# Optimization experiments

Hardware: AMD Instinct MI355X
Metric: run time of the kernel (lower is better)

The kernel has to match this reference:

```python
import jax, jax.numpy as jnp
import numpy as np

D_MODEL = 4096
NUM_EXPERTS = 16
HID_PER_EXPERT = 11008 // NUM_EXPERTS  # 688
NUM_SELECTS = 4
BALANCE_WEIGHT = 0.01
CV_EPS = 1e-10


def setup_inputs() -> dict:
    key = jax.random.key(0)
    ks = jax.random.split(key, 5)
    x = jax.random.normal(ks[0], (2, 2048, D_MODEL), dtype=jnp.float32)
    # gate network: Linear(input_size, num_experts, bias=False); stored as [D, E] for x @ W
    w_gate_net = jax.random.normal(ks[1], (D_MODEL, NUM_EXPERTS), dtype=jnp.float32) * (1.0 / np.sqrt(D_MODEL))
    # per-expert GLU weights (torch Linear convention [out, in]), stacked over experts
    s = 1.0 / np.sqrt(D_MODEL)
    w_g = jax.random.normal(ks[2], (NUM_EXPERTS, HID_PER_EXPERT, D_MODEL), dtype=jnp.float32) * s
    w_u = jax.random.normal(ks[3], (NUM_EXPERTS, HID_PER_EXPERT, D_MODEL), dtype=jnp.float32) * s
    w_d = jax.random.normal(ks[4], (NUM_EXPERTS, D_MODEL, HID_PER_EXPERT), dtype=jnp.float32) * (1.0 / np.sqrt(HID_PER_EXPERT))
    return {"x": x, "w_gate_net": w_gate_net, "w_g": w_g, "w_u": w_u, "w_d": w_d}


def _cv_squared(v):
    v = v.astype(jnp.float32)
    return jnp.var(v, ddof=1) / (jnp.mean(v) ** 2 + CV_EPS)


def reference(x, w_gate_net, w_g, w_u, w_d):
    B, S, D = x.shape
    E = w_g.shape[0]
    xt = x.reshape(-1, D)                      # [T, D]
    T = xt.shape[0]

    # --- TopKBalancedNoisyGate (eval path: no noise) ---
    logits = xt @ w_gate_net                   # [T, E]
    top_logits, top_idx = jax.lax.top_k(logits, NUM_SELECTS)   # [T, K]
    scores = jax.nn.softmax(top_logits.astype(jnp.float32), axis=-1).astype(logits.dtype)
    combine = jnp.zeros((T, E), dtype=logits.dtype)
    combine = combine.at[jnp.arange(T)[:, None], top_idx].set(scores)  # scatter topK scores
    importance = combine.sum(axis=0)           # [E]
    load = (combine > 0).sum(axis=0).astype(jnp.float32)
    balance_loss = (_cv_squared(importance) + _cv_squared(load)) * BALANCE_WEIGHT

    # --- UniversalCalculator with LinearGLUExperts (silu GLU, no bias) ---
    # dense per-expert compute; unrouted tokens have combine weight 0, so math matches
    # the gather/grouped-GEMM/scatter of the original exactly.
    g = jnp.einsum('td,ehd->teh', xt, w_g)     # [T, E, Hper]
    u = jnp.einsum('td,ehd->teh', xt, w_u)
    h = jax.nn.silu(g) * u * combine[:, :, None]  # multiply_gate_scores before down proj (bias-free => exact)
    y = jnp.einsum('teh,edh->td', h, w_d)      # [T, D]
    return y.reshape(B, S, -1), balance_loss
```

## Files before the change

kernel.cpp:

```cpp
#include <hip/hip_runtime.h>
#include <hip/hip_bf16.h>

#define D_MODEL 4096
#define NEXP    16
#define HID     688
#define HIDP    704
#define NSEL    4
#define NTOK    4096

typedef __attribute__((ext_vector_type(4))) float  f32x4;
typedef __attribute__((ext_vector_type(8))) short  bf16x8;

__device__ __forceinline__ short f2bf(float f) {
  __hip_bfloat16 h = __float2bfloat16(f);
  return __builtin_bit_cast(short, h);
}

__device__ __forceinline__ void gload16(const void* g, void* l) {
  __builtin_amdgcn_global_load_lds(
      (const __attribute__((address_space(1))) unsigned int*)g,
      (__attribute__((address_space(3))) unsigned int*)l, 16, 0, 0);
}

__global__ void zero_meta_kernel(int* counts, float* importance) {
  const int tid = threadIdx.x;
  if (tid < NEXP) counts[tid] = 0;
  else if (tid < 2 * NEXP) importance[tid - NEXP] = 0.f;
}

__global__ void zero_y_kernel(float* __restrict__ y) {
  const size_t i = (size_t)blockIdx.x * 256 + threadIdx.x;
  *(f32x4*)(y + i * 4) = f32x4{0.f, 0.f, 0.f, 0.f};
}

#define GC_CONV_BLOCKS 2048
__global__ __launch_bounds__(256) void gate_conv_kernel(
    const float* __restrict__ x, const float* __restrict__ wg,
    int* __restrict__ counts, float* __restrict__ importance,
    int* __restrict__ pair_tok, float* __restrict__ pair_scr,
    int* __restrict__ pair_rank, short* __restrict__ xb,
    const float* __restrict__ w_g, const float* __restrict__ w_u,
    short* __restrict__ gb, short* __restrict__ ub)
{
  __shared__ double red[4][NEXP];
  const int tid = threadIdx.x;

  if (blockIdx.x < GC_CONV_BLOCKS) {
    const size_t stride = (size_t)GC_CONV_BLOCKS * 256;
    const size_t n8 = (size_t)NEXP * HIDP * (D_MODEL / 8);
    for (size_t i = (size_t)blockIdx.x * 256 + tid; i < n8; i += stride) {
      const int c8  = (int)(i & 511);
      const int row = (int)((i >> 9) % HIDP);
      const int e   = (int)(i / (512 * HIDP));
      bf16x8 og, ou;
      if (row < HID) {
        const size_t so = ((size_t)e * HID + row) * D_MODEL + (size_t)c8 * 8;
        const f32x4 ga  = *(const f32x4*)(w_g + so);
        const f32x4 gbv = *(const f32x4*)(w_g + so + 4);
        const f32x4 ua  = *(const f32x4*)(w_u + so);
        const f32x4 ubv = *(const f32x4*)(w_u + so + 4);
        #pragma unroll
        for (int j = 0; j < 4; ++j) {
          og[j] = f2bf(ga[j]); og[4 + j] = f2bf(gbv[j]);
          ou[j] = f2bf(ua[j]); ou[4 + j] = f2bf(ubv[j]);
        }
      } else {
        #pragma unroll
        for (int j = 0; j < 8; ++j) { og[j] = 0; ou[j] = 0; }
      }
      *(bf16x8*)(gb + i * 8) = og;
      *(bf16x8*)(ub + i * 8) = ou;
    }
    return;
  }

  const int t = blockIdx.x - GC_CONV_BLOCKS;
  const float* xr = x + (size_t)t * D_MODEL;
  {
    short* xbr = xb + (size_t)t * D_MODEL;
    for (int i8 = tid; i8 < D_MODEL / 8; i8 += 256) {
      const f32x4 a = *(const f32x4*)(xr + i8 * 8);
      const f32x4 b = *(const f32x4*)(xr + i8 * 8 + 4);
      bf16x8 o;
      #pragma unroll
      for (int j = 0; j < 4; ++j) { o[j] = f2bf(a[j]); o[4 + j] = f2bf(b[j]); }
      *(bf16x8*)(xbr + i8 * 8) = o;
    }
  }

  double acc[NEXP];
  #pragma unroll
  for (int e = 0; e < NEXP; ++e) acc[e] = 0.0;

  for (int i = tid; i < D_MODEL; i += 256) {
    const float xv = xr[i];
    const f32x4* w = (const f32x4*)(wg + (size_t)i * NEXP);
    #pragma unroll
    for (int q = 0; q < 4; ++q) {
      const f32x4 wv = w[q];
      #pragma unroll
      for (int j = 0; j < 4; ++j) acc[q * 4 + j] += (double)xv * (double)wv[j];
    }
  }

  #pragma unroll
  for (int e = 0; e < NEXP; ++e) {
    double v = acc[e];
    #pragma unroll
    for (int off = 32; off > 0; off >>= 1) v += __shfl_xor(v, off, 64);
    acc[e] = v;
  }

  const int lane = tid & 63, wid = tid >> 6;
  if (lane == 0) {
    #pragma unroll
    for (int e = 0; e < NEXP; ++e) red[wid][e] = acc[e];
  }
  __syncthreads();

  if (tid == 0) {
    float lg[NEXP];
    #pragma unroll
    for (int e = 0; e < NEXP; ++e)
      lg[e] = (float)(red[0][e] + red[1][e] + red[2][e] + red[3][e]);

    int   idx[NSEL];
    float val[NSEL];
    unsigned used = 0;
    for (int k = 0; k < NSEL; ++k) {
      float best = -3.4e38f; int bi = 0;
      for (int e = 0; e < NEXP; ++e)
        if (!((used >> e) & 1u) && lg[e] > best) { best = lg[e]; bi = e; }
      idx[k] = bi; val[k] = best; used |= 1u << bi;
    }
    const float m = val[0];
    float ex[NSEL], s = 0.f;
    for (int k = 0; k < NSEL; ++k) { ex[k] = expf(val[k] - m); s += ex[k]; }
    for (int k = 0; k < NSEL; ++k) {
      const float sc = ex[k] / s;
      const int e = idx[k];
      const int pos = atomicAdd(&counts[e], 1);
      pair_tok[e * NTOK + pos]  = t;
      pair_scr[e * NTOK + pos]  = sc;
      pair_rank[e * NTOK + pos] = k;
      atomicAdd(&importance[e], sc);
    }
  }
}

__global__ void scan_loss_kernel(const int* __restrict__ counts,
                                 const float* __restrict__ importance,
                                 int* __restrict__ offs, float* __restrict__ loss_out)
{
  if (threadIdx.x != 0 || blockIdx.x != 0) return;
  int   c[NEXP]; float im[NEXP];
  for (int e = 0; e < NEXP; ++e) { c[e] = counts[e]; im[e] = importance[e]; }
  int o = 0;
  for (int e = 0; e < NEXP; ++e) { offs[e] = o; o += c[e]; }
  float mi = 0.f, ml = 0.f;
  for (int e = 0; e < NEXP; ++e) { mi += im[e]; ml += (float)c[e]; }
  mi /= NEXP; ml /= NEXP;
  float vi = 0.f, vl = 0.f;
  for (int e = 0; e < NEXP; ++e) {
    vi += (im[e] - mi) * (im[e] - mi);
    vl += ((float)c[e] - ml) * ((float)c[e] - ml);
  }
  vi /= (NEXP - 1); vl /= (NEXP - 1);
  const float loss = 0.01f * (vi / (mi * mi + 1e-10f) + vl / (ml * ml + 1e-10f));
  *loss_out = loss;
}

#define S1_CONV_BLOCKS 2048
__global__ __launch_bounds__(256, 4) void stage1_wd_kernel(
    const short* __restrict__ xb, const short* __restrict__ wgb,
    const short* __restrict__ wub, const int* __restrict__ counts,
    const int* __restrict__ offs, const int* __restrict__ pair_tok,
    const float* __restrict__ pair_scr, short* __restrict__ H,
    const float* __restrict__ w_d, short* __restrict__ wdb)
{
  __shared__ short ldsA[2][128 * 32];
  __shared__ short ldsG[2][64 * 32];
  __shared__ short ldsU[2][64 * 32];

  const int tid = threadIdx.x;

  if (blockIdx.x < S1_CONV_BLOCKS) {
    const size_t stride = (size_t)S1_CONV_BLOCKS * 256;
    const size_t n8 = (size_t)NEXP * D_MODEL * (HIDP / 8);
    for (size_t i = (size_t)blockIdx.x * 256 + tid; i < n8; i += stride) {
      const int c8  = (int)(i % 88);
      const int row = (int)((i / 88) & (D_MODEL - 1));
      const int e   = (int)(i / (88 * D_MODEL));
      bf16x8 o;
      if (c8 < 86) {
        const size_t so = ((size_t)e * D_MODEL + row) * HID + (size_t)c8 * 8;
        const f32x4 a = *(const f32x4*)(w_d + so);
        const f32x4 b = *(const f32x4*)(w_d + so + 4);
        #pragma unroll
        for (int j = 0; j < 4; ++j) { o[j] = f2bf(a[j]); o[4 + j] = f2bf(b[j]); }
      } else {
        #pragma unroll
        for (int j = 0; j < 8; ++j) o[j] = 0;
      }
      *(bf16x8*)(wdb + i * 8) = o;
    }
    return;
  }

  const int bid = blockIdx.x - S1_CONV_BLOCKS;
  const int ht  = bid >> 9;
  const int q   = bid & 511;
  const int xcd = q & 7;
  const int idx = q >> 3;
  const int e   = xcd * 2 + (idx & 1);
  const int mt  = idx >> 1;

  const int n_e = counts[e];
  const int m0  = mt * 128;
  if (m0 >= n_e) return;
  const int h0  = ht * 64;

  const int lane = tid & 63;
  const int wid  = tid >> 6;

  const short* srcA[2]; const short* srcG; const short* srcU;
  #pragma unroll
  for (int i = 0; i < 2; ++i) {
    const int c    = wid * 2 + i;
    const int row  = 16 * c + (lane >> 2);
    const int slot = (lane & 3) ^ ((row >> 1) & 3);
    int r = m0 + row; if (r >= n_e) r = n_e - 1;
    const int tok = pair_tok[e * NTOK + r];
    srcA[i] = xb + (size_t)tok * D_MODEL + slot * 8;
  }
  {
    const int c    = wid;
    const int row  = 16 * c + (lane >> 2);
    const int slot = (lane & 3) ^ ((row >> 1) & 3);
    const size_t rb = ((size_t)e * HIDP + h0 + row) * D_MODEL + slot * 8;
    srcG = wgb + rb;
    srcU = wub + rb;
  }

  const int wm = wid >> 1, wn = wid & 1;
  const int fr = lane & 15, fs = lane >> 4;
  const int so = (fs ^ ((fr >> 1) & 3)) * 8;

  f32x4 accg[4][2], accu[4][2];
  #pragma unroll
  for (int fi = 0; fi < 4; ++fi)
    #pragma unroll
    for (int fj = 0; fj < 2; ++fj) {
      accg[fi][fj] = f32x4{0.f, 0.f, 0.f, 0.f};
      accu[fi][fj] = f32x4{0.f, 0.f, 0.f, 0.f};
    }

  auto stage = [&](int kt, int b) {
    const int ko = kt * 32;
    #pragma unroll
    for (int i = 0; i < 2; ++i)
      gload16(srcA[i] + ko, &ldsA[b][(wid * 2 + i) * 512]);
    gload16(srcG + ko, &ldsG[b][wid * 512]);
    gload16(srcU + ko, &ldsU[b][wid * 512]);
  };

  auto compute = [&](int b) {
    const short* Ab = ldsA[b]; const short* Gb = ldsG[b]; const short* Ub = ldsU[b];
    bf16x8 af[4], bg[2], bu[2];
    #pragma unroll
    for (int fi = 0; fi < 4; ++fi)
      af[fi] = *(const bf16x8*)&Ab[(wm * 64 + fi * 16 + fr) * 32 + so];
    #pragma unroll
    for (int fj = 0; fj < 2; ++fj) {
      bg[fj] = *(const bf16x8*)&Gb[(wn * 32 + fj * 16 + fr) * 32 + so];
      bu[fj] = *(const bf16x8*)&Ub[(wn * 32 + fj * 16 + fr) * 32 + so];
    }
    #pragma unroll
    for (int fi = 0; fi < 4; ++fi)
      #pragma unroll
      for (int fj = 0; fj < 2; ++fj) {
        accg[fi][fj] = __builtin_amdgcn_mfma_f32_16x16x32_bf16(af[fi], bg[fj], accg[fi][fj], 0, 0, 0);
        accu[fi][fj] = __builtin_amdgcn_mfma_f32_16x16x32_bf16(af[fi], bu[fj], accu[fi][fj], 0, 0, 0);
      }
  };

  const int KT = D_MODEL / 32;
  stage(0, 0);
  for (int kt = 0; kt < KT; ++kt) {
    const int cur = kt & 1;
    __syncthreads();
    if (kt + 1 < KT) stage(kt + 1, cur ^ 1);
    compute(cur);
  }

  const int offs_e = offs[e];
  #pragma unroll
  for (int fi = 0; fi < 4; ++fi)
    #pragma unroll
    for (int fj = 0; fj < 2; ++fj)
      #pragma unroll
      for (int j = 0; j < 4; ++j) {
        const int r = m0 + wm * 64 + fi * 16 + fs * 4 + j;
        if (r < n_e) {
          const int c = h0 + wn * 32 + fj * 16 + fr;
          const float sc = pair_scr[e * NTOK + r];
          const float g  = accg[fi][fj][j];
          const float u  = accu[fi][fj][j];
          const float hv = (g / (1.f + expf(-g))) * u * sc;
          H[(size_t)(offs_e + r) * HIDP + c] = f2bf(hv);
        }
      }
}

__global__ __launch_bounds__(256, 4) void stage2s_kernel(
    const short* __restrict__ H, const short* __restrict__ wdb,
    const int* __restrict__ counts, const int* __restrict__ offs,
    const int* __restrict__ pair_tok, const int* __restrict__ pair_rank,
    float* __restrict__ Yk)
{
  const int bid = blockIdx.x;
  const int dt  = bid >> 9;
  const int q   = bid & 511;
  const int xcd = q & 7;
  const int idx = q >> 3;
  const int e   = xcd * 2 + (idx & 1);
  const int mt  = idx >> 1;

  const int n_e = counts[e];
  const int m0  = mt * 128;
  if (m0 >= n_e) return;
  const int d0  = dt * 128;

  __shared__ short ldsA[2][128 * 32];
  __shared__ short ldsB[2][128 * 32];

  const int tid  = threadIdx.x;
  const int lane = tid & 63;
  const int wid  = tid >> 6;
  const int offs_e = offs[e];

  const short* srcA[2]; const short* srcB[2];
  #pragma unroll
  for (int i = 0; i < 2; ++i) {
    const int c    = wid * 2 + i;
    const int row  = 16 * c + (lane >> 2);
    const int slot = (lane & 3) ^ ((row >> 1) & 3);
    int r = m0 + row; if (r >= n_e) r = n_e - 1;
    srcA[i] = H + (size_t)(offs_e + r) * HIDP + slot * 8;
    srcB[i] = wdb + ((size_t)e * D_MODEL + d0 + row) * HIDP + slot * 8;
  }

  const int wm = wid >> 1, wn = wid & 1;
  const int fr = lane & 15, fs = lane >> 4;
  const int so = (fs ^ ((fr >> 1) & 3)) * 8;

  f32x4 acc[4][4];
  #pragma unroll
  for (int fi = 0; fi < 4; ++fi)
    #pragma unroll
    for (int fj = 0; fj < 4; ++fj) acc[fi][fj] = f32x4{0.f, 0.f, 0.f, 0.f};

  auto stage = [&](int kt, int b) {
    const int ko = kt * 32;
    #pragma unroll
    for (int i = 0; i < 2; ++i) {
      gload16(srcA[i] + ko, &ldsA[b][(wid * 2 + i) * 512]);
      gload16(srcB[i] + ko, &ldsB[b][(wid * 2 + i) * 512]);
    }
  };

  auto compute = [&](int b) {
    const short* Ab = ldsA[b]; const short* Bb = ldsB[b];
    bf16x8 af[4], bb[4];
    #pragma unroll
    for (int fi = 0; fi < 4; ++fi)
      af[fi] = *(const bf16x8*)&Ab[(wm * 64 + fi * 16 + fr) * 32 + so];
    #pragma unroll
    for (int fj = 0; fj < 4; ++fj)
      bb[fj] = *(const bf16x8*)&Bb[(wn * 64 + fj * 16 + fr) * 32 + so];
    #pragma unroll
    for (int fi = 0; fi < 4; ++fi)
      #pragma unroll
      for (int fj = 0; fj < 4; ++fj)
        acc[fi][fj] = __builtin_amdgcn_mfma_f32_16x16x32_bf16(af[fi], bb[fj], acc[fi][fj], 0, 0, 0);
  };

  const int KT = HIDP / 32;
  stage(0, 0);
  for (int kt = 0; kt < KT; ++kt) {
    const int cur = kt & 1;
    __syncthreads();
    if (kt + 1 < KT) stage(kt + 1, cur ^ 1);
    compute(cur);
  }

  #pragma unroll
  for (int fi = 0; fi < 4; ++fi)
    #pragma unroll
    for (int j = 0; j < 4; ++j) {
      const int r = m0 + wm * 64 + fi * 16 + fs * 4 + j;
      if (r < n_e) {
        const int tok = pair_tok[e * NTOK + r];
        const int rk  = pair_rank[e * NTOK + r];
        float* yr = Yk + ((size_t)rk * NTOK + tok) * D_MODEL + d0 + wn * 64 + fr;
        #pragma unroll
        for (int fj = 0; fj < 4; ++fj)
          yr[fj * 16] = acc[fi][fj][j];
      }
    }
}

__global__ __launch_bounds__(256) void reduce_y_kernel(const float* __restrict__ Yk,
                                                       float* __restrict__ y) {
  const size_t i = ((size_t)blockIdx.x * 256 + threadIdx.x) * 4;
  const size_t P = (size_t)NTOK * D_MODEL;
  f32x4 s = *(const f32x4*)(Yk + i);
  s += *(const f32x4*)(Yk + P + i);
  s += *(const f32x4*)(Yk + 2 * P + i);
  s += *(const f32x4*)(Yk + 3 * P + i);
  *(f32x4*)(y + i) = s;
}

__global__ __launch_bounds__(256, 4) void stage2a_kernel(
    const short* __restrict__ H, const short* __restrict__ wdb,
    const int* __restrict__ counts, const int* __restrict__ offs,
    const int* __restrict__ pair_tok, float* __restrict__ y)
{
  const int bid = blockIdx.x;
  const int dt  = bid >> 9;
  const int q   = bid & 511;
  const int xcd = q & 7;
  const int idx = q >> 3;
  const int e   = xcd * 2 + (idx & 1);
  const int mt  = idx >> 1;

  const int n_e = counts[e];
  const int m0  = mt * 128;
  if (m0 >= n_e) return;
  const int d0  = dt * 128;

  __shared__ short ldsA[2][128 * 32];
  __shared__ short ldsB[2][128 * 32];

  const int tid  = threadIdx.x;
  const int lane = tid & 63;
  const int wid  = tid >> 6;
  const int offs_e = offs[e];

  const short* srcA[2]; const short* srcB[2];
  #pragma unroll
  for (int i = 0; i < 2; ++i) {
    const int c    = wid * 2 + i;
    const int row  = 16 * c + (lane >> 2);
    const int slot = (lane & 3) ^ ((row >> 1) & 3);
    int r = m0 + row; if (r >= n_e) r = n_e - 1;
    srcA[i] = H + (size_t)(offs_e + r) * HIDP + slot * 8;
    srcB[i] = wdb + ((size_t)e * D_MODEL + d0 + row) * HIDP + slot * 8;
  }

  const int wm = wid >> 1, wn = wid & 1;
  const int fr = lane & 15, fs = lane >> 4;
  const int so = (fs ^ ((fr >> 1) & 3)) * 8;

  f32x4 acc[4][4];
  #pragma unroll
  for (int fi = 0; fi < 4; ++fi)
    #pragma unroll
    for (int fj = 0; fj < 4; ++fj) acc[fi][fj] = f32x4{0.f, 0.f, 0.f, 0.f};

  auto stage = [&](int kt, int b) {
    const int ko = kt * 32;
    #pragma unroll
    for (int i = 0; i < 2; ++i) {
      gload16(srcA[i] + ko, &ldsA[b][(wid * 2 + i) * 512]);
      gload16(srcB[i] + ko, &ldsB[b][(wid * 2 + i) * 512]);
    }
  };

  auto compute = [&](int b) {
    const short* Ab = ldsA[b]; const short* Bb = ldsB[b];
    bf16x8 af[4], bb[4];
    #pragma unroll
    for (int fi = 0; fi < 4; ++fi)
      af[fi] = *(const bf16x8*)&Ab[(wm * 64 + fi * 16 + fr) * 32 + so];
    #pragma unroll
    for (int fj = 0; fj < 4; ++fj)
      bb[fj] = *(const bf16x8*)&Bb[(wn * 64 + fj * 16 + fr) * 32 + so];
    #pragma unroll
    for (int fi = 0; fi < 4; ++fi)
      #pragma unroll
      for (int fj = 0; fj < 4; ++fj)
        acc[fi][fj] = __builtin_amdgcn_mfma_f32_16x16x32_bf16(af[fi], bb[fj], acc[fi][fj], 0, 0, 0);
  };

  const int KT = HIDP / 32;
  stage(0, 0);
  for (int kt = 0; kt < KT; ++kt) {
    const int cur = kt & 1;
    __syncthreads();
    if (kt + 1 < KT) stage(kt + 1, cur ^ 1);
    compute(cur);
  }

  #pragma unroll
  for (int fi = 0; fi < 4; ++fi)
    #pragma unroll
    for (int j = 0; j < 4; ++j) {
      const int r = m0 + wm * 64 + fi * 16 + fs * 4 + j;
      if (r < n_e) {
        const int tok = pair_tok[e * NTOK + r];
        float* yr = y + (size_t)tok * D_MODEL + d0 + wn * 64 + fr;
        #pragma unroll
        for (int fj = 0; fj < 4; ++fj)
          atomicAdd(yr + fj * 16, acc[fi][fj][j]);
      }
    }
}

extern "C" void kernel_launch(void* const* d_in, const int* in_sizes, int n_in,
                              void* d_out, int out_size, void* d_ws, size_t ws_size,
                              hipStream_t stream) {
  const float* x     = (const float*)d_in[0];
  const float* wgate = (const float*)d_in[1];
  const float* w_g   = (const float*)d_in[2];
  const float* w_u   = (const float*)d_in[3];
  const float* w_d   = (const float*)d_in[4];

  float* y        = (float*)d_out;
  float* loss_out = y + (size_t)NTOK * D_MODEL;

  char* ws = (char*)d_ws;
  int*   counts     = (int*)ws;
  int*   offs       = counts + 16;
  float* importance = (float*)(counts + 32);
  int*   pair_tok   = (int*)(ws + 256);
  float* pair_scr   = (float*)(ws + 256 + (size_t)NEXP * NTOK * 4);
  int*   pair_rank  = (int*)(ws + 256 + (size_t)2 * NEXP * NTOK * 4);
  short* H          = (short*)(ws + 256 + (size_t)3 * NEXP * NTOK * 4);

  const size_t H_BYTES = (size_t)NTOK * NSEL * HIDP * 2;
  short* xbuf = (short*)((char*)H + H_BYTES);
  short* wgb  = xbuf + (size_t)NTOK * D_MODEL;
  short* wub  = wgb + (size_t)NEXP * HIDP * D_MODEL;
  short* wdb  = wub + (size_t)NEXP * HIDP * D_MODEL;
  float* Yk   = (float*)(wdb + (size_t)NEXP * HIDP * D_MODEL);

  const size_t NEED_STORE = ((char*)(Yk + (size_t)NSEL * NTOK * D_MODEL)) - ws;
  const bool store_path = ws_size >= NEED_STORE;

  hipLaunchKernelGGL(zero_meta_kernel, dim3(1), dim3(64), 0, stream, counts, importance);
  hipLaunchKernelGGL(gate_conv_kernel, dim3(GC_CONV_BLOCKS + NTOK), dim3(256), 0, stream,
                     x, wgate, counts, importance, pair_tok, pair_scr, pair_rank, xbuf,
                     w_g, w_u, wgb, wub);
  hipLaunchKernelGGL(scan_loss_kernel, dim3(1), dim3(64), 0, stream,
                     counts, importance, offs, loss_out);
  hipLaunchKernelGGL(stage1_wd_kernel, dim3(S1_CONV_BLOCKS + 11 * 512), dim3(256), 0, stream,
                     xbuf, wgb, wub, counts, offs, pair_tok, pair_scr, H, w_d, wdb);

  if (store_path) {
    hipLaunchKernelGGL(stage2s_kernel, dim3(32 * 512), dim3(256), 0, stream,
                       H, wdb, counts, offs, pair_tok, pair_rank, Yk);
    hipLaunchKernelGGL(reduce_y_kernel, dim3(NTOK * D_MODEL / 4 / 256), dim3(256), 0, stream,
                       Yk, y);
  } else {
    hipLaunchKernelGGL(zero_y_kernel, dim3(16384), dim3(256), 0, stream, y);
    hipLaunchKernelGGL(stage2a_kernel, dim3(32 * 512), dim3(256), 0, stream,
                       H, wdb, counts, offs, pair_tok, y);
  }
}
```

Before: 912.3 us.

## Load weight operands directly to registers and interleave conversion blocks with compute

Both GEMM stages now load the weight (B) fragments straight from global memory into registers, prefetching one k-step ahead, and no longer stage them through LDS. Only the gathered activation tile still goes through double-buffered LDS, which cuts LDS traffic and footprint. The weight-conversion blocks are also interleaved with compute blocks in the grid (every 3rd block in the gate kernel, every 4th in stage1), so conversion and compute run concurrently instead of in separate phases. The cost is uncoalesced per-lane 16-byte global loads for the weights, and per-step global load latency that is hidden only by a single register prefetch.

```diff
diff --git a/kernel.cpp b/kernel.cpp
--- a/kernel.cpp
+++ b/kernel.cpp
@@ -33,7 +33,6 @@
   *(f32x4*)(y + i * 4) = f32x4{0.f, 0.f, 0.f, 0.f};
 }
 
-#define GC_CONV_BLOCKS 2048
 __global__ __launch_bounds__(256) void gate_conv_kernel(
     const float* __restrict__ x, const float* __restrict__ wg,
     int* __restrict__ counts, float* __restrict__ importance,
@@ -44,11 +43,12 @@
 {
   __shared__ double red[4][NEXP];
   const int tid = threadIdx.x;
-
-  if (blockIdx.x < GC_CONV_BLOCKS) {
-    const size_t stride = (size_t)GC_CONV_BLOCKS * 256;
+  const int b3  = blockIdx.x / 3;
+
+  if (blockIdx.x % 3 == 2) {
+    const size_t stride = (size_t)2048 * 256;
     const size_t n8 = (size_t)NEXP * HIDP * (D_MODEL / 8);
-    for (size_t i = (size_t)blockIdx.x * 256 + tid; i < n8; i += stride) {
+    for (size_t i = (size_t)b3 * 256 + tid; i < n8; i += stride) {
       const int c8  = (int)(i & 511);
       const int row = (int)((i >> 9) % HIDP);
       const int e   = (int)(i / (512 * HIDP));
@@ -74,7 +74,7 @@
     return;
   }
 
-  const int t = blockIdx.x - GC_CONV_BLOCKS;
+  const int t = blockIdx.x - b3;
   const float* xr = x + (size_t)t * D_MODEL;
   {
     short* xbr = xb + (size_t)t * D_MODEL;
@@ -170,7 +170,6 @@
   *loss_out = loss;
 }
 
-#define S1_CONV_BLOCKS 2048
 __global__ __launch_bounds__(256, 4) void stage1_wd_kernel(
     const short* __restrict__ xb, const short* __restrict__ wgb,
     const short* __restrict__ wub, const int* __restrict__ counts,
@@ -179,15 +178,13 @@
     const float* __restrict__ w_d, short* __restrict__ wdb)
 {
   __shared__ short ldsA[2][128 * 32];
-  __shared__ short ldsG[2][64 * 32];
-  __shared__ short ldsU[2][64 * 32];
-
   const int tid = threadIdx.x;
 
-  if (blockIdx.x < S1_CONV_BLOCKS) {
-    const size_t stride = (size_t)S1_CONV_BLOCKS * 256;
+  if ((blockIdx.x & 3) == 0) {
+    const int cb = blockIdx.x >> 2;
+    const size_t stride = (size_t)2048 * 256;
     const size_t n8 = (size_t)NEXP * D_MODEL * (HIDP / 8);
-    for (size_t i = (size_t)blockIdx.x * 256 + tid; i < n8; i += stride) {
+    for (size_t i = (size_t)cb * 256 + tid; i < n8; i += stride) {
       const int c8  = (int)(i % 88);
       const int row = (int)((i / 88) & (D_MODEL - 1));
       const int e   = (int)(i / (88 * D_MODEL));
@@ -207,9 +204,10 @@
     return;
   }
 
-  const int bid = blockIdx.x - S1_CONV_BLOCKS;
-  const int ht  = bid >> 9;
-  const int q   = bid & 511;
+  const int sid = blockIdx.x - (blockIdx.x >> 2) - 1;
+  if (sid >= 11 * 512) return;
+  const int ht  = sid >> 9;
+  const int q   = sid & 511;
   const int xcd = q & 7;
   const int idx = q >> 3;
   const int e   = xcd * 2 + (idx & 1);
@@ -223,7 +221,7 @@
   const int lane = tid & 63;
   const int wid  = tid >> 6;
 
-  const short* srcA[2]; const short* srcG; const short* srcU;
+  const short* srcA[2];
   #pragma unroll
   for (int i = 0; i < 2; ++i) {
     const int c    = wid * 2 + i;
@@ -233,19 +231,20 @@
     const int tok = pair_tok[e * NTOK + r];
     srcA[i] = xb + (size_t)tok * D_MODEL + slot * 8;
   }
-  {
-    const int c    = wid;
-    const int row  = 16 * c + (lane >> 2);
-    const int slot = (lane & 3) ^ ((row >> 1) & 3);
-    const size_t rb = ((size_t)e * HIDP + h0 + row) * D_MODEL + slot * 8;
-    srcG = wgb + rb;
-    srcU = wub + rb;
-  }
 
   const int wm = wid >> 1, wn = wid & 1;
   const int fr = lane & 15, fs = lane >> 4;
   const int so = (fs ^ ((fr >> 1) & 3)) * 8;
 
+  const short* pg[2]; const short* pu[2];
+  #pragma unroll
+  for (int fj = 0; fj < 2; ++fj) {
+    const int hr = h0 + wn * 32 + fj * 16 + fr;
+    const size_t rb = ((size_t)e * HIDP + hr) * D_MODEL + fs * 8;
+    pg[fj] = wgb + rb;
+    pu[fj] = wub + rb;
+  }
+
   f32x4 accg[4][2], accu[4][2];
   #pragma unroll
   for (int fi = 0; fi < 4; ++fi)
@@ -255,26 +254,27 @@
       accu[fi][fj] = f32x4{0.f, 0.f, 0.f, 0.f};
     }
 
-  auto stage = [&](int kt, int b) {
+  auto stageA = [&](int kt, int b) {
     const int ko = kt * 32;
     #pragma unroll
     for (int i = 0; i < 2; ++i)
       gload16(srcA[i] + ko, &ldsA[b][(wid * 2 + i) * 512]);
-    gload16(srcG + ko, &ldsG[b][wid * 512]);
-    gload16(srcU + ko, &ldsU[b][wid * 512]);
   };
 
-  auto compute = [&](int b) {
-    const short* Ab = ldsA[b]; const short* Gb = ldsG[b]; const short* Ub = ldsU[b];
-    bf16x8 af[4], bg[2], bu[2];
+  bf16x8 bg[2], bu[2];
+  #pragma unroll
+  for (int fj = 0; fj < 2; ++fj) { bg[fj] = *(const bf16x8*)(pg[fj]); bu[fj] = *(const bf16x8*)(pu[fj]); }
+  stageA(0, 0);
+
+  const int KT = D_MODEL / 32;
+  for (int kt = 0; kt < KT; ++kt) {
+    const int cur = kt & 1;
+    __syncthreads();
+    if (kt + 1 < KT) stageA(kt + 1, cur ^ 1);
+    bf16x8 af[4];
     #pragma unroll
     for (int fi = 0; fi < 4; ++fi)
-      af[fi] = *(const bf16x8*)&Ab[(wm * 64 + fi * 16 + fr) * 32 + so];
-    #pragma unroll
-    for (int fj = 0; fj < 2; ++fj) {
-      bg[fj] = *(const bf16x8*)&Gb[(wn * 32 + fj * 16 + fr) * 32 + so];
-      bu[fj] = *(const bf16x8*)&Ub[(wn * 32 + fj * 16 + fr) * 32 + so];
-    }
+      af[fi] = *(const bf16x8*)&ldsA[cur][(wm * 64 + fi * 16 + fr) * 32 + so];
     #pragma unroll
     for (int fi = 0; fi < 4; ++fi)
       #pragma unroll
@@ -282,15 +282,14 @@
         accg[fi][fj] = __builtin_amdgcn_mfma_f32_16x16x32_bf16(af[fi], bg[fj], accg[fi][fj], 0, 0, 0);
         accu[fi][fj] = __builtin_amdgcn_mfma_f32_16x16x32_bf16(af[fi], bu[fj], accu[fi][fj], 0, 0, 0);
       }
-  };
-
-  const int KT = D_MODEL / 32;
-  stage(0, 0);
-  for (int kt = 0; kt < KT; ++kt) {
-    const int cur = kt & 1;
-    __syncthreads();
-    if (kt + 1 < KT) stage(kt + 1, cur ^ 1);
-    compute(cur);
+    if (kt + 1 < KT) {
+      const int ko = (kt + 1) * 32;
+      #pragma unroll
+      for (int fj = 0; fj < 2; ++fj) {
+        bg[fj] = *(const bf16x8*)(pg[fj] + ko);
+        bu[fj] = *(const bf16x8*)(pu[fj] + ko);
+      }
+    }
   }
 
   const int offs_e = offs[e];
@@ -332,14 +331,13 @@
   const int d0  = dt * 128;
 
   __shared__ short ldsA[2][128 * 32];
-  __shared__ short ldsB[2][128 * 32];
 
   const int tid  = threadIdx.x;
   const int lane = tid & 63;
   const int wid  = tid >> 6;
   const int offs_e = offs[e];
 
-  const short* srcA[2]; const short* srcB[2];
+  const short* srcA[2];
   #pragma unroll
   for (int i = 0; i < 2; ++i) {
     const int c    = wid * 2 + i;
@@ -347,51 +345,56 @@
     const int slot = (lane & 3) ^ ((row >> 1) & 3);
     int r = m0 + row; if (r >= n_e) r = n_e - 1;
     srcA[i] = H + (size_t)(offs_e + r) * HIDP + slot * 8;
-    srcB[i] = wdb + ((size_t)e * D_MODEL + d0 + row) * HIDP + slot * 8;
   }
 
   const int wm = wid >> 1, wn = wid & 1;
   const int fr = lane & 15, fs = lane >> 4;
   const int so = (fs ^ ((fr >> 1) & 3)) * 8;
 
+  const short* pb[4];
+  #pragma unroll
+  for (int fj = 0; fj < 4; ++fj) {
+    const int drow = d0 + wn * 64 + fj * 16 + fr;
+    pb[fj] = wdb + ((size_t)e * D_MODEL + drow) * HIDP + fs * 8;
+  }
+
   f32x4 acc[4][4];
   #pragma unroll
   for (int fi = 0; fi < 4; ++fi)
     #pragma unroll
     for (int fj = 0; fj < 4; ++fj) acc[fi][fj] = f32x4{0.f, 0.f, 0.f, 0.f};
 
-  auto stage = [&](int kt, int b) {
+  auto stageA = [&](int kt, int b) {
     const int ko = kt * 32;
     #pragma unroll
-    for (int i = 0; i < 2; ++i) {
+    for (int i = 0; i < 2; ++i)
       gload16(srcA[i] + ko, &ldsA[b][(wid * 2 + i) * 512]);
-      gload16(srcB[i] + ko, &ldsB[b][(wid * 2 + i) * 512]);
-    }
   };
 
-  auto compute = [&](int b) {
-    const short* Ab = ldsA[b]; const short* Bb = ldsB[b];
-    bf16x8 af[4], bb[4];
-    #pragma unroll
-    for (int fi = 0; fi < 4; ++fi)
-      af[fi] = *(const bf16x8*)&Ab[(wm * 64 + fi * 16 + fr) * 32 + so];
-    #pragma unroll
-    for (int fj = 0; fj < 4; ++fj)
-      bb[fj] = *(const bf16x8*)&Bb[(wn * 64 + fj * 16 + fr) * 32 + so];
-    #pragma unroll
-    for (int fi = 0; fi < 4; ++fi)
-      #pragma unroll
-      for (int fj = 0; fj < 4; ++fj)
-        acc[fi][fj] = __builtin_amdgcn_mfma_f32_16x16x32_bf16(af[fi], bb[fj], acc[fi][fj], 0, 0, 0);
-  };
+  bf16x8 bb[4];
+  #pragma unroll
+  for (int fj = 0; fj < 4; ++fj) bb[fj] = *(const bf16x8*)(pb[fj]);
+  stageA(0, 0);
 
   const int KT = HIDP / 32;
-  stage(0, 0);
   for (int kt = 0; kt < KT; ++kt) {
     const int cur = kt & 1;
     __syncthreads();
-    if (kt + 1 < KT) stage(kt + 1, cur ^ 1);
-    compute(cur);
+    if (kt + 1 < KT) stageA(kt + 1, cur ^ 1);
+    bf16x8 af[4];
+    #pragma unroll
+    for (int fi = 0; fi < 4; ++fi)
+      af[fi] = *(const bf16x8*)&ldsA[cur][(wm * 64 + fi * 16 + fr) * 32 + so];
+    #pragma unroll
+    for (int fi = 0; fi < 4; ++fi)
+      #pragma unroll
+      for (int fj = 0; fj < 4; ++fj)
+        acc[fi][fj] = __builtin_amdgcn_mfma_f32_16x16x32_bf16(af[fi], bb[fj], acc[fi][fj], 0, 0, 0);
+    if (kt + 1 < KT) {
+      const int ko = (kt + 1) * 32;
+      #pragma unroll
+      for (int fj = 0; fj < 4; ++fj) bb[fj] = *(const bf16x8*)(pb[fj] + ko);
+    }
   }
 
   #pragma unroll
@@ -440,14 +443,13 @@
   const int d0  = dt * 128;
 
   __shared__ short ldsA[2][128 * 32];
-  __shared__ short ldsB[2][128 * 32];
 
   const int tid  = threadIdx.x;
   const int lane = tid & 63;
   const int wid  = tid >> 6;
   const int offs_e = offs[e];
 
-  const short* srcA[2]; const short* srcB[2];
+  const short* srcA[2];
   #pragma unroll
   for (int i = 0; i < 2; ++i) {
     const int c    = wid * 2 + i;
@@ -455,51 +457,56 @@
     const int slot = (lane & 3) ^ ((row >> 1) & 3);
     int r = m0 + row; if (r >= n_e) r = n_e - 1;
     srcA[i] = H + (size_t)(offs_e + r) * HIDP + slot * 8;
-    srcB[i] = wdb + ((size_t)e * D_MODEL + d0 + row) * HIDP + slot * 8;
   }
 
   const int wm = wid >> 1, wn = wid & 1;
   const int fr = lane & 15, fs = lane >> 4;
   const int so = (fs ^ ((fr >> 1) & 3)) * 8;
 
+  const short* pb[4];
+  #pragma unroll
+  for (int fj = 0; fj < 4; ++fj) {
+    const int drow = d0 + wn * 64 + fj * 16 + fr;
+    pb[fj] = wdb + ((size_t)e * D_MODEL + drow) * HIDP + fs * 8;
+  }
+
   f32x4 acc[4][4];
   #pragma unroll
   for (int fi = 0; fi < 4; ++fi)
     #pragma unroll
     for (int fj = 0; fj < 4; ++fj) acc[fi][fj] = f32x4{0.f, 0.f, 0.f, 0.f};
 
-  auto stage = [&](int kt, int b) {
+  auto stageA = [&](int kt, int b) {
     const int ko = kt * 32;
     #pragma unroll
-    for (int i = 0; i < 2; ++i) {
+    for (int i = 0; i < 2; ++i)
       gload16(srcA[i] + ko, &ldsA[b][(wid * 2 + i) * 512]);
-      gload16(srcB[i] + ko, &ldsB[b][(wid * 2 + i) * 512]);
-    }
   };
 
-  auto compute = [&](int b) {
-    const short* Ab = ldsA[b]; const short* Bb = ldsB[b];
-    bf16x8 af[4], bb[4];
-    #pragma unroll
-    for (int fi = 0; fi < 4; ++fi)
-      af[fi] = *(const bf16x8*)&Ab[(wm * 64 + fi * 16 + fr) * 32 + so];
-    #pragma unroll
-    for (int fj = 0; fj < 4; ++fj)
-      bb[fj] = *(const bf16x8*)&Bb[(wn * 64 + fj * 16 + fr) * 32 + so];
-    #pragma unroll
-    for (int fi = 0; fi < 4; ++fi)
-      #pragma unroll
-      for (int fj = 0; fj < 4; ++fj)
-        acc[fi][fj] = __builtin_amdgcn_mfma_f32_16x16x32_bf16(af[fi], bb[fj], acc[fi][fj], 0, 0, 0);
-  };
+  bf16x8 bb[4];
+  #pragma unroll
+  for (int fj = 0; fj < 4; ++fj) bb[fj] = *(const bf16x8*)(pb[fj]);
+  stageA(0, 0);
 
   const int KT = HIDP / 32;
-  stage(0, 0);
   for (int kt = 0; kt < KT; ++kt) {
     const int cur = kt & 1;
     __syncthreads();
-    if (kt + 1 < KT) stage(kt + 1, cur ^ 1);
-    compute(cur);
+    if (kt + 1 < KT) stageA(kt + 1, cur ^ 1);
+    bf16x8 af[4];
+    #pragma unroll
+    for (int fi = 0; fi < 4; ++fi)
+      af[fi] = *(const bf16x8*)&ldsA[cur][(wm * 64 + fi * 16 + fr) * 32 + so];
+    #pragma unroll
+    for (int fi = 0; fi < 4; ++fi)
+      #pragma unroll
+      for (int fj = 0; fj < 4; ++fj)
+        acc[fi][fj] = __builtin_amdgcn_mfma_f32_16x16x32_bf16(af[fi], bb[fj], acc[fi][fj], 0, 0, 0);
+    if (kt + 1 < KT) {
+      const int ko = (kt + 1) * 32;
+      #pragma unroll
+      for (int fj = 0; fj < 4; ++fj) bb[fj] = *(const bf16x8*)(pb[fj] + ko);
+    }
   }
 
   #pragma unroll
@@ -549,12 +556,12 @@
   const bool store_path = ws_size >= NEED_STORE;
 
   hipLaunchKernelGGL(zero_meta_kernel, dim3(1), dim3(64), 0, stream, counts, importance);
-  hipLaunchKernelGGL(gate_conv_kernel, dim3(GC_CONV_BLOCKS + NTOK), dim3(256), 0, stream,
+  hipLaunchKernelGGL(gate_conv_kernel, dim3(6144), dim3(256), 0, stream,
                      x, wgate, counts, importance, pair_tok, pair_scr, pair_rank, xbuf,
                      w_g, w_u, wgb, wub);
   hipLaunchKernelGGL(scan_loss_kernel, dim3(1), dim3(64), 0, stream,
                      counts, importance, offs, loss_out);
-  hipLaunchKernelGGL(stage1_wd_kernel, dim3(S1_CONV_BLOCKS + 11 * 512), dim3(256), 0, stream,
+  hipLaunchKernelGGL(stage1_wd_kernel, dim3(8192), dim3(256), 0, stream,
                      xbuf, wgb, wub, counts, offs, pair_tok, pair_scr, H, w_d, wdb);
 
   if (store_path) {
```

New measurement: 1.271 ms. 1.39x slower.

## Move w_d conversion into gate kernel and store per-slot partials in bf16

Applied to the files above, without the earlier changes.

The fp32-to-bf16 conversion of w_d moves from the stage-1 GEMM launch into the gate/convert kernel. Its blocks are interleaved by blockIdx mod 4 with w_g/w_u conversion and per-token gating, so the conversion traffic overlaps with gating and the stage-1 GEMM runs alone. The per-selection partial outputs Yk are now written as bf16 instead of fp32, which halves store and reduce traffic. The cost is extra rounding error in the summed output.

```diff
diff --git a/kernel.cpp b/kernel.cpp
--- a/kernel.cpp
+++ b/kernel.cpp
@@ -16,6 +16,11 @@
   return __builtin_bit_cast(short, h);
 }
 
+__device__ __forceinline__ float bf2f(short s) {
+  const unsigned u = ((unsigned)(unsigned short)s) << 16;
+  return __builtin_bit_cast(float, u);
+}
+
 __device__ __forceinline__ void gload16(const void* g, void* l) {
   __builtin_amdgcn_global_load_lds(
       (const __attribute__((address_space(1))) unsigned int*)g,
@@ -33,22 +38,24 @@
   *(f32x4*)(y + i * 4) = f32x4{0.f, 0.f, 0.f, 0.f};
 }
 
-#define GC_CONV_BLOCKS 2048
 __global__ __launch_bounds__(256) void gate_conv_kernel(
     const float* __restrict__ x, const float* __restrict__ wg,
     int* __restrict__ counts, float* __restrict__ importance,
     int* __restrict__ pair_tok, float* __restrict__ pair_scr,
     int* __restrict__ pair_rank, short* __restrict__ xb,
     const float* __restrict__ w_g, const float* __restrict__ w_u,
-    short* __restrict__ gb, short* __restrict__ ub)
+    short* __restrict__ gb, short* __restrict__ ub,
+    const float* __restrict__ w_d, short* __restrict__ wdb)
 {
   __shared__ double red[4][NEXP];
   const int tid = threadIdx.x;
-
-  if (blockIdx.x < GC_CONV_BLOCKS) {
-    const size_t stride = (size_t)GC_CONV_BLOCKS * 256;
+  const int r4  = blockIdx.x & 3;
+  const int b4  = blockIdx.x >> 2;
+
+  if (r4 == 0) {
+    const size_t stride = (size_t)2048 * 256;
     const size_t n8 = (size_t)NEXP * HIDP * (D_MODEL / 8);
-    for (size_t i = (size_t)blockIdx.x * 256 + tid; i < n8; i += stride) {
+    for (size_t i = (size_t)b4 * 256 + tid; i < n8; i += stride) {
       const int c8  = (int)(i & 511);
       const int row = (int)((i >> 9) % HIDP);
       const int e   = (int)(i / (512 * HIDP));
@@ -74,7 +81,30 @@
     return;
   }
 
-  const int t = blockIdx.x - GC_CONV_BLOCKS;
+  if (r4 == 1) {
+    const size_t stride = (size_t)2048 * 256;
+    const size_t n8 = (size_t)NEXP * D_MODEL * (HIDP / 8);
+    for (size_t i = (size_t)b4 * 256 + tid; i < n8; i += stride) {
+      const int c8  = (int)(i % 88);
+      const int row = (int)((i / 88) & (D_MODEL - 1));
+      const int e   = (int)(i / (88 * D_MODEL));
+      bf16x8 o;
+      if (c8 < 86) {
+        const size_t so = ((size_t)e * D_MODEL + row) * HID + (size_t)c8 * 8;
+        const f32x4 a = *(const f32x4*)(w_d + so);
+        const f32x4 b = *(const f32x4*)(w_d + so + 4);
+        #pragma unroll
+        for (int j = 0; j < 4; ++j) { o[j] = f2bf(a[j]); o[4 + j] = f2bf(b[j]); }
+      } else {
+        #pragma unroll
+        for (int j = 0; j < 8; ++j) o[j] = 0;
+      }
+      *(bf16x8*)(wdb + i * 8) = o;
+    }
+    return;
+  }
+
+  const int t = b4 * 2 + (r4 - 2);
   const float* xr = x + (size_t)t * D_MODEL;
   {
     short* xbr = xb + (size_t)t * D_MODEL;
@@ -170,44 +200,13 @@
   *loss_out = loss;
 }
 
-#define S1_CONV_BLOCKS 2048
-__global__ __launch_bounds__(256, 4) void stage1_wd_kernel(
+__global__ __launch_bounds__(256, 4) void stage1b_kernel(
     const short* __restrict__ xb, const short* __restrict__ wgb,
     const short* __restrict__ wub, const int* __restrict__ counts,
     const int* __restrict__ offs, const int* __restrict__ pair_tok,
-    const float* __restrict__ pair_scr, short* __restrict__ H,
-    const float* __restrict__ w_d, short* __restrict__ wdb)
+    const float* __restrict__ pair_scr, short* __restrict__ H)
 {
-  __shared__ short ldsA[2][128 * 32];
-  __shared__ short ldsG[2][64 * 32];
-  __shared__ short ldsU[2][64 * 32];
-
-  const int tid = threadIdx.x;
-
-  if (blockIdx.x < S1_CONV_BLOCKS) {
-    const size_t stride = (size_t)S1_CONV_BLOCKS * 256;
-    const size_t n8 = (size_t)NEXP * D_MODEL * (HIDP / 8);
-    for (size_t i = (size_t)blockIdx.x * 256 + tid; i < n8; i += stride) {
-      const int c8  = (int)(i % 88);
-      const int row = (int)((i / 88) & (D_MODEL - 1));
-      const int e   = (int)(i / (88 * D_MODEL));
-      bf16x8 o;
-      if (c8 < 86) {
-        const size_t so = ((size_t)e * D_MODEL + row) * HID + (size_t)c8 * 8;
-        const f32x4 a = *(const f32x4*)(w_d + so);
-        const f32x4 b = *(const f32x4*)(w_d + so + 4);
-        #pragma unroll
-        for (int j = 0; j < 4; ++j) { o[j] = f2bf(a[j]); o[4 + j] = f2bf(b[j]); }
-      } else {
-        #pragma unroll
-        for (int j = 0; j < 8; ++j) o[j] = 0;
-      }
-      *(bf16x8*)(wdb + i * 8) = o;
-    }
-    return;
-  }
-
-  const int bid = blockIdx.x - S1_CONV_BLOCKS;
+  const int bid = blockIdx.x;
   const int ht  = bid >> 9;
   const int q   = bid & 511;
   const int xcd = q & 7;
@@ -220,6 +219,11 @@
   if (m0 >= n_e) return;
   const int h0  = ht * 64;
 
+  __shared__ short ldsA[2][128 * 32];
+  __shared__ short ldsG[2][64 * 32];
+  __shared__ short ldsU[2][64 * 32];
+
+  const int tid  = threadIdx.x;
   const int lane = tid & 63;
   const int wid  = tid >> 6;
 
@@ -316,7 +320,7 @@
     const short* __restrict__ H, const short* __restrict__ wdb,
     const int* __restrict__ counts, const int* __restrict__ offs,
     const int* __restrict__ pair_tok, const int* __restrict__ pair_rank,
-    float* __restrict__ Yk)
+    short* __restrict__ Yk)
 {
   const int bid = blockIdx.x;
   const int dt  = bid >> 9;
@@ -402,23 +406,30 @@
       if (r < n_e) {
         const int tok = pair_tok[e * NTOK + r];
         const int rk  = pair_rank[e * NTOK + r];
-        float* yr = Yk + ((size_t)rk * NTOK + tok) * D_MODEL + d0 + wn * 64 + fr;
+        short* yr = Yk + ((size_t)rk * NTOK + tok) * D_MODEL + d0 + wn * 64 + fr;
         #pragma unroll
         for (int fj = 0; fj < 4; ++fj)
-          yr[fj * 16] = acc[fi][fj][j];
+          yr[fj * 16] = f2bf(acc[fi][fj][j]);
       }
     }
 }
 
-__global__ __launch_bounds__(256) void reduce_y_kernel(const float* __restrict__ Yk,
+__global__ __launch_bounds__(256) void reduce_y_kernel(const short* __restrict__ Yk,
                                                        float* __restrict__ y) {
-  const size_t i = ((size_t)blockIdx.x * 256 + threadIdx.x) * 4;
+  const size_t i = ((size_t)blockIdx.x * 256 + threadIdx.x) * 8;
   const size_t P = (size_t)NTOK * D_MODEL;
-  f32x4 s = *(const f32x4*)(Yk + i);
-  s += *(const f32x4*)(Yk + P + i);
-  s += *(const f32x4*)(Yk + 2 * P + i);
-  s += *(const f32x4*)(Yk + 3 * P + i);
-  *(f32x4*)(y + i) = s;
+  const bf16x8 a = *(const bf16x8*)(Yk + i);
+  const bf16x8 b = *(const bf16x8*)(Yk + P + i);
+  const bf16x8 c = *(const bf16x8*)(Yk + 2 * P + i);
+  const bf16x8 d = *(const bf16x8*)(Yk + 3 * P + i);
+  f32x4 lo, hi;
+  #pragma unroll
+  for (int j = 0; j < 4; ++j) {
+    lo[j] = bf2f(a[j]) + bf2f(b[j]) + bf2f(c[j]) + bf2f(d[j]);
+    hi[j] = bf2f(a[4 + j]) + bf2f(b[4 + j]) + bf2f(c[4 + j]) + bf2f(d[4 + j]);
+  }
+  *(f32x4*)(y + i)     = lo;
+  *(f32x4*)(y + i + 4) = hi;
 }
 
 __global__ __launch_bounds__(256, 4) void stage2a_kernel(
@@ -543,24 +554,24 @@
   short* wgb  = xbuf + (size_t)NTOK * D_MODEL;
   short* wub  = wgb + (size_t)NEXP * HIDP * D_MODEL;
   short* wdb  = wub + (size_t)NEXP * HIDP * D_MODEL;
-  float* Yk   = (float*)(wdb + (size_t)NEXP * HIDP * D_MODEL);
+  short* Yk   = wdb + (size_t)NEXP * HIDP * D_MODEL;
 
   const size_t NEED_STORE = ((char*)(Yk + (size_t)NSEL * NTOK * D_MODEL)) - ws;
   const bool store_path = ws_size >= NEED_STORE;
 
   hipLaunchKernelGGL(zero_meta_kernel, dim3(1), dim3(64), 0, stream, counts, importance);
-  hipLaunchKernelGGL(gate_conv_kernel, dim3(GC_CONV_BLOCKS + NTOK), dim3(256), 0, stream,
+  hipLaunchKernelGGL(gate_conv_kernel, dim3(8192), dim3(256), 0, stream,
                      x, wgate, counts, importance, pair_tok, pair_scr, pair_rank, xbuf,
-                     w_g, w_u, wgb, wub);
+                     w_g, w_u, wgb, wub, w_d, wdb);
   hipLaunchKernelGGL(scan_loss_kernel, dim3(1), dim3(64), 0, stream,
                      counts, importance, offs, loss_out);
-  hipLaunchKernelGGL(stage1_wd_kernel, dim3(S1_CONV_BLOCKS + 11 * 512), dim3(256), 0, stream,
-                     xbuf, wgb, wub, counts, offs, pair_tok, pair_scr, H, w_d, wdb);
+  hipLaunchKernelGGL(stage1b_kernel, dim3(11 * 512), dim3(256), 0, stream,
+                     xbuf, wgb, wub, counts, offs, pair_tok, pair_scr, H);
 
   if (store_path) {
     hipLaunchKernelGGL(stage2s_kernel, dim3(32 * 512), dim3(256), 0, stream,
                        H, wdb, counts, offs, pair_tok, pair_rank, Yk);
-    hipLaunchKernelGGL(reduce_y_kernel, dim3(NTOK * D_MODEL / 4 / 256), dim3(256), 0, stream,
+    hipLaunchKernelGGL(reduce_y_kernel, dim3(NTOK * D_MODEL / 8 / 256), dim3(256), 0, stream,
                        Yk, y);
   } else {
     hipLaunchKernelGGL(zero_y_kernel, dim3(16384), dim3(256), 0, stream, y);
```

Measured after the change: 756.4 us. 1.21x faster.
